# Optimization experiments

Hardware: AMD Instinct MI355X
Metric: run time of the kernel (lower is better)

Reference implementation:

```python
import jax, jax.numpy as jnp
import numpy as np

N_NODES = 100000
N_EDGES = 625000
D_IN = 128
D_OUT = 128


def setup_inputs() -> dict:
    key = jax.random.key(0)
    k1, k2, k3, k4 = jax.random.split(key, 4)
    embeds = jax.random.normal(k1, (N_NODES, D_IN), dtype=jnp.float32)
    weight = jax.random.normal(k2, (D_IN, D_OUT), dtype=jnp.float32)
    # COO sparse adjacency: row 0 = destination node, row 1 = source node
    edge_index = jax.random.randint(k3, (2, N_DGES := N_EDGES), 0, N_NODES, dtype=jnp.int32)
    edge_vals = jax.random.uniform(k4, (N_EDGES,), dtype=jnp.float32)
    return {"embeds": embeds, "weight": weight, "edge_index": edge_index, "edge_vals": edge_vals}


def reference(embeds, weight, edge_index, edge_vals):
    # support = embeds @ W  -> [N, D_OUT]
    support = jnp.matmul(embeds, weight)
    dst, src = edge_index[0], edge_index[1]
    # spmm: out[d] = sum_{e: dst[e]==d} vals[e] * support[src[e]]
    msgs = edge_vals[:, None] * support[src]  # [E, D_OUT]
    output = jax.ops.segment_sum(msgs, dst, num_segments=embeds.shape[0])
    return output
```

## Files before the change

kernel.cpp:

```cpp
#include <hip/hip_runtime.h>

#define D 128
#define CB 256
#define CB_SHIFT 8
#define NB_MAX 512
#define CAP 4096

typedef __attribute__((ext_vector_type(8))) short short8;
typedef __attribute__((ext_vector_type(4))) float f32x4;

__device__ inline ushort f2bf(float f) {
    uint u = __float_as_uint(f);
    uint r = (u + 0x7FFFu + ((u >> 16) & 1u)) >> 16;
    return (ushort)r;
}

__device__ inline uint cvtpk(float lo, float hi) {
    uint r;
    asm("v_cvt_pk_bf16_f32 %0, %1, %2" : "=v"(r) : "v"(lo), "v"(hi));
    return r;
}


__global__ __launch_bounds__(256) void init_kernel(int* __restrict__ cnt,
                                                   const float* __restrict__ W,
                                                   ushort* __restrict__ wT) {
    const int t = threadIdx.x;
    if (blockIdx.x == 0) { cnt[t] = 0; cnt[t + 256] = 0; }
    const int gt = blockIdx.x * 256 + t;
    if (gt < D * D) { int r = gt >> 7, c = gt & 127; wT[c * D + r] = f2bf(W[gt]); }
}


__global__ void zero_f4_kernel(float4* __restrict__ out, int n4) {
    int i = blockIdx.x * blockDim.x + threadIdx.x;
    int stride = gridDim.x * blockDim.x;
    float4 z = make_float4(0.f, 0.f, 0.f, 0.f);
    for (; i < n4; i += stride) out[i] = z;
}


__global__ __launch_bounds__(512) void gemm_part(const float* __restrict__ embeds,
                                                 const ushort* __restrict__ wT,
                                                 ushort* __restrict__ support, int N,
                                                 const int* __restrict__ dst,
                                                 const int* __restrict__ srcp,
                                                 const float* __restrict__ vals,
                                                 int* __restrict__ cnt,
                                                 int2* __restrict__ pay1, int E, int npart) {
    __shared__ ushort bLds[D * D];
    __shared__ int phist[NB_MAX];
    __shared__ int pbase[NB_MAX];
    const int t = threadIdx.x;

    if ((int)blockIdx.x < npart) {
        const int ntile = (E + 2047) >> 11;
        for (int tile = blockIdx.x; tile < ntile; tile += npart) {
            const int e0 = tile << 11;
            if (t < NB_MAX) phist[t] = 0;
            __syncthreads();

            int bk[4], rk[4];
            #pragma unroll
            for (int j = 0; j < 4; ++j) {
                int e = e0 + j * 512 + t;
                bk[j] = -1;
                if (e < E) {
                    bk[j] = dst[e] >> CB_SHIFT;
                    rk[j] = atomicAdd(&phist[bk[j]], 1);
                }
            }
            __syncthreads();

            if (t < NB_MAX)
                pbase[t] = phist[t] ? (t * CAP + atomicAdd(&cnt[t], phist[t])) : 0;
            __syncthreads();

            #pragma unroll
            for (int j = 0; j < 4; ++j) {
                int e = e0 + j * 512 + t;
                if (e >= E) continue;
                int d = dst[e];
                int pos = pbase[bk[j]] + rk[j];
                if (pos < (bk[j] + 1) * CAP) {
                    int key = ((d & (CB - 1)) << 17) | srcp[e];
                    pay1[pos] = make_int2(key, __float_as_int(vals[e]));
                }
            }
            __syncthreads();
        }
        return;
    }

    const int gbid = blockIdx.x - npart;
    const int ngemm = gridDim.x - npart;
    const int w = t >> 6;
    const int l = t & 63;
    const int kgrp = l >> 4;
    const int lan15 = l & 15;

    #pragma unroll
    for (int c = 0; c < 4; ++c) {
        int chunk = c * 512 + t;
        int byteoff = chunk * 16;
        int n = byteoff >> 8;
        int dstoff = byteoff ^ ((n & 7) << 4);
        *(float4*)((char*)bLds + dstoff) = *(const float4*)((const char*)wT + byteoff);
    }
    __syncthreads();

    const int ntiles = (N + 127) >> 7;

    for (int tile = gbid; tile < ntiles; tile += ngemm) {
        const int row0 = tile << 7;
        const int grow = row0 + w * 16 + lan15;
        const bool valid = grow < N;
        const float* arow = embeds + (size_t)grow * D + kgrp * 8;

        float4 pf[8];
        if (valid) {
            #pragma unroll
            for (int ks = 0; ks < 4; ++ks) {
                pf[2 * ks]     = *(const float4*)(arow + ks * 32);
                pf[2 * ks + 1] = *(const float4*)(arow + ks * 32 + 4);
            }
        } else {
            #pragma unroll
            for (int j = 0; j < 8; ++j) pf[j] = make_float4(0.f, 0.f, 0.f, 0.f);
        }

        f32x4 acc[8];
        #pragma unroll
        for (int ct = 0; ct < 8; ++ct) acc[ct] = (f32x4)0.0f;

        #pragma unroll
        for (int ks = 0; ks < 4; ++ks) {
            union { uint4 u; short8 s; } cv;
            const float4 f0 = pf[2 * ks], f1 = pf[2 * ks + 1];
            cv.u.x = cvtpk(f0.x, f0.y);
            cv.u.y = cvtpk(f0.z, f0.w);
            cv.u.z = cvtpk(f1.x, f1.y);
            cv.u.w = cvtpk(f1.z, f1.w);
            const short8 af = cv.s;

            const int kbyte = ks * 64 + kgrp * 16;
            #pragma unroll
            for (int ct = 0; ct < 8; ++ct) {
                const int n = ct * 16 + lan15;
                const int boff = (n * 256 + kbyte) ^ ((n & 7) << 4);
                short8 bfr = *(const short8*)((const char*)bLds + boff);
                acc[ct] = __builtin_amdgcn_mfma_f32_16x16x32_bf16(af, bfr, acc[ct], 0, 0, 0);
            }
        }

        #pragma unroll
        for (int r = 0; r < 4; ++r) {
            const int orow = row0 + w * 16 + kgrp * 4 + r;
            if (orow < N) {
                ushort* srow = &support[(size_t)orow * D + lan15];
                #pragma unroll
                for (int cp = 0; cp < 4; ++cp) {
                    uint u = cvtpk(acc[2 * cp][r], acc[2 * cp + 1][r]);
                    srow[(2 * cp) * 16] = (ushort)u;
                    srow[(2 * cp + 1) * 16] = (ushort)(u >> 16);
                }
            }
        }
    }
}


__global__ __launch_bounds__(256) void finefill2(const int2* __restrict__ pay1,
                                                 const int* __restrict__ cnt,
                                                 int2* __restrict__ ranges,
                                                 int2* __restrict__ pay,
                                                 int N, int nb) {
    __shared__ int lcnt[CB];
    __shared__ int bs[CB];
    __shared__ int lofs[CB];
    const int t = threadIdx.x;

    for (int b = blockIdx.x; b < nb; b += gridDim.x) {
        const int beg = b * CAP;
        const int end = beg + min(cnt[b], CAP);
        const int d0 = b << CB_SHIFT;

        lcnt[t] = 0;
        __syncthreads();
        for (int i = beg + t; i < end; i += 256)
            atomicAdd(&lcnt[((unsigned)pay1[i].x) >> 17], 1);
        __syncthreads();

        const int c = lcnt[t];
        bs[t] = c;
        __syncthreads();
        for (int off = 1; off < 256; off <<= 1) {
            int x = (t >= off) ? bs[t - off] : 0;
            __syncthreads();
            bs[t] += x;
            __syncthreads();
        }
        const int run = bs[t] - c + beg;
        if (d0 + t < N) ranges[d0 + t] = make_int2(run, run + c);
        lofs[t] = run;
        __syncthreads();

        for (int i = beg + t; i < end; i += 256) {
            int2 p = pay1[i];
            int dl = ((unsigned)p.x) >> 17;
            int pos = atomicAdd(&lofs[dl], 1);
            pay[pos] = make_int2(p.x & 0x1FFFF, p.y);
        }
        __syncthreads();
    }
}


#define EDGE_MAC(P, M)                                          \
    do {                                                        \
        const float v_ = __int_as_float((P).y);                 \
        acc[0] += v_ * __uint_as_float(((M).x & 0xFFFFu) << 16);\
        acc[1] += v_ * __uint_as_float((M).x & 0xFFFF0000u);    \
        acc[2] += v_ * __uint_as_float(((M).y & 0xFFFFu) << 16);\
        acc[3] += v_ * __uint_as_float((M).y & 0xFFFF0000u);    \
        acc[4] += v_ * __uint_as_float(((M).z & 0xFFFFu) << 16);\
        acc[5] += v_ * __uint_as_float((M).z & 0xFFFF0000u);    \
        acc[6] += v_ * __uint_as_float(((M).w & 0xFFFFu) << 16);\
        acc[7] += v_ * __uint_as_float((M).w & 0xFFFF0000u);    \
    } while (0)

__global__ __launch_bounds__(256, 8) void gather_kernel(const ushort* __restrict__ support,
                                                        const int2* __restrict__ ranges,
                                                        const int2* __restrict__ pay,
                                                        float* __restrict__ out, int N) {
    const int gid = (blockIdx.x * 256 + threadIdx.x) >> 4;
    const int sl = threadIdx.x & 15;
    if (gid >= N) return;

    const int2 rg = ranges[gid];
    const int beg = rg.x;
    const int end = rg.y;

    float acc[8];
    #pragma unroll
    for (int j = 0; j < 8; ++j) acc[j] = 0.f;

    int i = beg;
    for (; i + 3 < end; i += 4) {
        const int2 p0 = pay[i], p1 = pay[i + 1], p2 = pay[i + 2], p3 = pay[i + 3];
        const uint4 m0 = *(const uint4*)&support[(size_t)p0.x * D + sl * 8];
        const uint4 m1 = *(const uint4*)&support[(size_t)p1.x * D + sl * 8];
        const uint4 m2 = *(const uint4*)&support[(size_t)p2.x * D + sl * 8];
        const uint4 m3 = *(const uint4*)&support[(size_t)p3.x * D + sl * 8];
        EDGE_MAC(p0, m0); EDGE_MAC(p1, m1); EDGE_MAC(p2, m2); EDGE_MAC(p3, m3);
    }
    for (; i + 1 < end; i += 2) {
        const int2 p0 = pay[i], p1 = pay[i + 1];
        const uint4 m0 = *(const uint4*)&support[(size_t)p0.x * D + sl * 8];
        const uint4 m1 = *(const uint4*)&support[(size_t)p1.x * D + sl * 8];
        EDGE_MAC(p0, m0); EDGE_MAC(p1, m1);
    }
    if (i < end) {
        const int2 p0 = pay[i];
        const uint4 m0 = *(const uint4*)&support[(size_t)p0.x * D + sl * 8];
        EDGE_MAC(p0, m0);
    }

    float* o = &out[(size_t)gid * D + sl * 8];
    *(float4*)o       = make_float4(acc[0], acc[1], acc[2], acc[3]);
    *(float4*)(o + 4) = make_float4(acc[4], acc[5], acc[6], acc[7]);
}


__global__ __launch_bounds__(256) void scatter_kernel(const ushort* __restrict__ support,
                                                      const int* __restrict__ dst,
                                                      const int* __restrict__ src,
                                                      const float* __restrict__ vals,
                                                      float* __restrict__ out, int E) {
    const long long tid = (long long)blockIdx.x * blockDim.x + threadIdx.x;
    const int e = (int)(tid >> 6);
    if (e >= E) return;
    const int c = ((int)tid & 63) * 2;

    const int s = src[e];
    const int d = dst[e];
    const float v = vals[e];

    const uint m = *(const uint*)&support[(size_t)s * D + c];
    const float mx = __uint_as_float((m & 0xFFFFu) << 16);
    const float my = __uint_as_float(m & 0xFFFF0000u);
    atomicAdd(&out[(size_t)d * D + c + 0], v * mx);
    atomicAdd(&out[(size_t)d * D + c + 1], v * my);
}


static inline char* align256(char* p) {
    return (char*)(((uintptr_t)p + 255) & ~(uintptr_t)255);
}

extern "C" void kernel_launch(void* const* d_in, const int* in_sizes, int n_in,
                              void* d_out, int out_size, void* d_ws, size_t ws_size,
                              hipStream_t stream) {
    const float* embeds = (const float*)d_in[0];
    const float* W      = (const float*)d_in[1];
    const int*   eidx   = (const int*)d_in[2];
    const float* vals   = (const float*)d_in[3];

    const int N = in_sizes[0] / D;
    const int E = in_sizes[3];
    const int* dstp = eidx;
    const int* srcp = eidx + E;

    float* out = (float*)d_out;

    const int nb = (N + CB - 1) / CB;

    char* p = (char*)d_ws;
    ushort* support = (ushort*)p;  p = align256(p + (size_t)N * D * 2);
    ushort* wT      = (ushort*)p;  p = align256(p + (size_t)D * D * 2);
    int2* ranges    = (int2*)p;    p = align256(p + (size_t)N * 8);
    int* cnt        = (int*)p;     p = align256(p + NB_MAX * 4);
    int2* pay       = (int2*)p;    p = align256(p + (size_t)nb * CAP * 8);
    int2* pay1      = (int2*)p;    p = align256(p + (size_t)nb * CAP * 8);
    const size_t needed = (size_t)(p - (char*)d_ws);

    const bool two_level = (N <= (1 << 17)) && (nb <= NB_MAX) &&
                           ((long long)E * 2 <= (long long)nb * CAP) &&
                           (ws_size >= needed);

    if (two_level) {
        init_kernel<<<64, 256, 0, stream>>>(cnt, W, wT);

        const int ntile = (E + 2047) / 2048;
        const int npart = ntile < 512 ? ntile : 512;
        gemm_part<<<npart + 512, 512, 0, stream>>>(embeds, wT, support, N,
                                                   dstp, srcp, vals, cnt, pay1, E, npart);

        finefill2<<<nb, 256, 0, stream>>>(pay1, cnt, ranges, pay, N, nb);
        gather_kernel<<<(N * 16 + 255) / 256, 256, 0, stream>>>(support, ranges, pay, out, N);
    } else {
        init_kernel<<<64, 256, 0, stream>>>(cnt, W, wT);
        gemm_part<<<512, 512, 0, stream>>>(embeds, wT, support, N,
                                           dstp, srcp, vals, cnt, pay1, E, 0);
        zero_f4_kernel<<<2048, 256, 0, stream>>>((float4*)out, out_size / 4);
        const long long nthreads = (long long)E * 64;
        const int blocks = (int)((nthreads + 255) / 256);
        scatter_kernel<<<blocks, 256, 0, stream>>>(support, dstp, srcp, vals, out, E);
    }
}
```

Baseline: 74.62 us.

## Use one GEMM tile per block, larger partition tiles, and wider LDS swizzle

The GEMM blocks now each handle exactly one 128-row tile, launched as ntiles blocks, instead of grid-striding over tiles with 512 blocks. The partition phase processes 8192-edge tiles per block and takes slots through shared-memory atomics on pbase rather than keeping per-thread ranks in registers. The LDS swizzle for the weight matrix changes from a 3-bit to a 4-bit XOR pattern to cut bank conflicts. In exchange, each block now loads the full weight matrix into LDS for a single tile, and the slot order within a bucket becomes nondeterministic.

Result: no change. 74.59 us (-0.0%).

```diff
diff --git a/kernel.cpp b/kernel.cpp
--- a/kernel.cpp
+++ b/kernel.cpp
@@ -5,6 +5,7 @@
 #define CB_SHIFT 8
 #define NB_MAX 512
 #define CAP 4096
+#define PT 8192
 
 typedef __attribute__((ext_vector_type(8))) short short8;
 typedef __attribute__((ext_vector_type(4))) float f32x4;
@@ -54,36 +55,28 @@
     const int t = threadIdx.x;
 
     if ((int)blockIdx.x < npart) {
-        const int ntile = (E + 2047) >> 11;
+        const int ntile = (E + PT - 1) / PT;
         for (int tile = blockIdx.x; tile < ntile; tile += npart) {
-            const int e0 = tile << 11;
+            const int e0 = tile * PT;
+            const int e1 = min(e0 + PT, E);
+
             if (t < NB_MAX) phist[t] = 0;
             __syncthreads();
 
-            int bk[4], rk[4];
-            #pragma unroll
-            for (int j = 0; j < 4; ++j) {
-                int e = e0 + j * 512 + t;
-                bk[j] = -1;
-                if (e < E) {
-                    bk[j] = dst[e] >> CB_SHIFT;
-                    rk[j] = atomicAdd(&phist[bk[j]], 1);
-                }
-            }
+            for (int e = e0 + t; e < e1; e += 512)
+                atomicAdd(&phist[dst[e] >> CB_SHIFT], 1);
             __syncthreads();
 
             if (t < NB_MAX)
                 pbase[t] = phist[t] ? (t * CAP + atomicAdd(&cnt[t], phist[t])) : 0;
             __syncthreads();
 
-            #pragma unroll
-            for (int j = 0; j < 4; ++j) {
-                int e = e0 + j * 512 + t;
-                if (e >= E) continue;
-                int d = dst[e];
-                int pos = pbase[bk[j]] + rk[j];
-                if (pos < (bk[j] + 1) * CAP) {
-                    int key = ((d & (CB - 1)) << 17) | srcp[e];
+            for (int e = e0 + t; e < e1; e += 512) {
+                const int d = dst[e];
+                const int b = d >> CB_SHIFT;
+                const int pos = atomicAdd(&pbase[b], 1);
+                if (pos < (b + 1) * CAP) {
+                    const int key = ((d & (CB - 1)) << 17) | srcp[e];
                     pay1[pos] = make_int2(key, __float_as_int(vals[e]));
                 }
             }
@@ -92,8 +85,10 @@
         return;
     }
 
-    const int gbid = blockIdx.x - npart;
-    const int ngemm = gridDim.x - npart;
+    const int tile = blockIdx.x - npart;
+    const int ntiles = (N + 127) >> 7;
+    if (tile >= ntiles) return;
+
     const int w = t >> 6;
     const int l = t & 63;
     const int kgrp = l >> 4;
@@ -104,66 +99,62 @@
         int chunk = c * 512 + t;
         int byteoff = chunk * 16;
         int n = byteoff >> 8;
-        int dstoff = byteoff ^ ((n & 7) << 4);
+        int dstoff = byteoff ^ ((n & 15) << 4);
         *(float4*)((char*)bLds + dstoff) = *(const float4*)((const char*)wT + byteoff);
     }
     __syncthreads();
 
-    const int ntiles = (N + 127) >> 7;
-
-    for (int tile = gbid; tile < ntiles; tile += ngemm) {
-        const int row0 = tile << 7;
-        const int grow = row0 + w * 16 + lan15;
-        const bool valid = grow < N;
-        const float* arow = embeds + (size_t)grow * D + kgrp * 8;
-
-        float4 pf[8];
-        if (valid) {
-            #pragma unroll
-            for (int ks = 0; ks < 4; ++ks) {
-                pf[2 * ks]     = *(const float4*)(arow + ks * 32);
-                pf[2 * ks + 1] = *(const float4*)(arow + ks * 32 + 4);
-            }
-        } else {
-            #pragma unroll
-            for (int j = 0; j < 8; ++j) pf[j] = make_float4(0.f, 0.f, 0.f, 0.f);
-        }
-
-        f32x4 acc[8];
-        #pragma unroll
-        for (int ct = 0; ct < 8; ++ct) acc[ct] = (f32x4)0.0f;
-
+    const int row0 = tile << 7;
+    const int grow = row0 + w * 16 + lan15;
+    const bool valid = grow < N;
+    const float* arow = embeds + (size_t)grow * D + kgrp * 8;
+
+    float4 pf[8];
+    if (valid) {
         #pragma unroll
         for (int ks = 0; ks < 4; ++ks) {
-            union { uint4 u; short8 s; } cv;
-            const float4 f0 = pf[2 * ks], f1 = pf[2 * ks + 1];
-            cv.u.x = cvtpk(f0.x, f0.y);
-            cv.u.y = cvtpk(f0.z, f0.w);
-            cv.u.z = cvtpk(f1.x, f1.y);
-            cv.u.w = cvtpk(f1.z, f1.w);
-            const short8 af = cv.s;
-
-            const int kbyte = ks * 64 + kgrp * 16;
+            pf[2 * ks]     = *(const float4*)(arow + ks * 32);
+            pf[2 * ks + 1] = *(const float4*)(arow + ks * 32 + 4);
+        }
+    } else {
+        #pragma unroll
+        for (int j = 0; j < 8; ++j) pf[j] = make_float4(0.f, 0.f, 0.f, 0.f);
+    }
+
+    f32x4 acc[8];
+    #pragma unroll
+    for (int ct = 0; ct < 8; ++ct) acc[ct] = (f32x4)0.0f;
+
+    #pragma unroll
+    for (int ks = 0; ks < 4; ++ks) {
+        union { uint4 u; short8 s; } cv;
+        const float4 f0 = pf[2 * ks], f1 = pf[2 * ks + 1];
+        cv.u.x = cvtpk(f0.x, f0.y);
+        cv.u.y = cvtpk(f0.z, f0.w);
+        cv.u.z = cvtpk(f1.x, f1.y);
+        cv.u.w = cvtpk(f1.z, f1.w);
+        const short8 af = cv.s;
+
+        const int kbyte = ks * 64 + kgrp * 16;
+        #pragma unroll
+        for (int ct = 0; ct < 8; ++ct) {
+            const int n = ct * 16 + lan15;
+            const int boff = (n * 256 + kbyte) ^ ((n & 15) << 4);
+            short8 bfr = *(const short8*)((const char*)bLds + boff);
+            acc[ct] = __builtin_amdgcn_mfma_f32_16x16x32_bf16(af, bfr, acc[ct], 0, 0, 0);
+        }
+    }
+
+    #pragma unroll
+    for (int r = 0; r < 4; ++r) {
+        const int orow = row0 + w * 16 + kgrp * 4 + r;
+        if (orow < N) {
+            ushort* srow = &support[(size_t)orow * D + lan15];
             #pragma unroll
-            for (int ct = 0; ct < 8; ++ct) {
-                const int n = ct * 16 + lan15;
-                const int boff = (n * 256 + kbyte) ^ ((n & 7) << 4);
-                short8 bfr = *(const short8*)((const char*)bLds + boff);
-                acc[ct] = __builtin_amdgcn_mfma_f32_16x16x32_bf16(af, bfr, acc[ct], 0, 0, 0);
-            }
-        }
-
-        #pragma unroll
-        for (int r = 0; r < 4; ++r) {
-            const int orow = row0 + w * 16 + kgrp * 4 + r;
-            if (orow < N) {
-                ushort* srow = &support[(size_t)orow * D + lan15];
-                #pragma unroll
-                for (int cp = 0; cp < 4; ++cp) {
-                    uint u = cvtpk(acc[2 * cp][r], acc[2 * cp + 1][r]);
-                    srow[(2 * cp) * 16] = (ushort)u;
-                    srow[(2 * cp + 1) * 16] = (ushort)(u >> 16);
-                }
+            for (int cp = 0; cp < 4; ++cp) {
+                uint u = cvtpk(acc[2 * cp][r], acc[2 * cp + 1][r]);
+                srow[(2 * cp) * 16] = (ushort)u;
+                srow[(2 * cp + 1) * 16] = (ushort)(u >> 16);
             }
         }
     }
@@ -314,6 +305,7 @@
     float* out = (float*)d_out;
 
     const int nb = (N + CB - 1) / CB;
+    const int ntiles = (N + 127) >> 7;
 
     char* p = (char*)d_ws;
     ushort* support = (ushort*)p;  p = align256(p + (size_t)N * D * 2);
@@ -331,17 +323,19 @@
     if (two_level) {
         init_kernel<<<64, 256, 0, stream>>>(cnt, W, wT);
 
-        const int ntile = (E + 2047) / 2048;
-        const int npart = ntile < 512 ? ntile : 512;
-        gemm_part<<<npart + 512, 512, 0, stream>>>(embeds, wT, support, N,
-                                                   dstp, srcp, vals, cnt, pay1, E, npart);
+        const int ptile = (E + PT - 1) / PT;
+        const int npart = ptile < 512 ? ptile : 512;
+        int total = npart + ntiles;
+        if (total > 1024 && npart + 512 < total) total = (npart + ntiles);
+        gemm_part<<<npart + ntiles, 512, 0, stream>>>(embeds, wT, support, N,
+                                                      dstp, srcp, vals, cnt, pay1, E, npart);
 
         finefill2<<<nb, 256, 0, stream>>>(pay1, cnt, ranges, pay, N, nb);
         gather_kernel<<<(N * 16 + 255) / 256, 256, 0, stream>>>(support, ranges, pay, out, N);
     } else {
         init_kernel<<<64, 256, 0, stream>>>(cnt, W, wT);
-        gemm_part<<<512, 512, 0, stream>>>(embeds, wT, support, N,
-                                           dstp, srcp, vals, cnt, pay1, E, 0);
+        gemm_part<<<ntiles, 512, 0, stream>>>(embeds, wT, support, N,
+                                              dstp, srcp, vals, cnt, pay1, E, 0);
         zero_f4_kernel<<<2048, 256, 0, stream>>>((float4*)out, out_size / 4);
         const long long nthreads = (long long)E * 64;
         const int blocks = (int)((nthreads + 255) / 256);
```

## Split fused GEMM/partition kernel into separate partition and one-tile-per-block GEMM kernels

Applied to the files above, without the earlier changes.

Replaces the combined gemm_part launch, where some blocks partitioned edges and others ran persistent GEMM loops, with two kernels launched back to back: a 256-thread partition kernel with one block per tile, and a GEMM kernel with one block per 128-row tile. The LDS swizzle for the weight tile also changes from an XOR over 8 rows to one over 16 rows, to cut bank conflicts. The GEMM blocks no longer run beside the partition work. In exchange there is an extra launch, and each GEMM block now reloads the weight tile into LDS.

Result: slower. 80.90 us (+8.4%).

```diff
diff --git a/kernel.cpp b/kernel.cpp
--- a/kernel.cpp
+++ b/kernel.cpp
@@ -5,6 +5,7 @@
 #define CB_SHIFT 8
 #define NB_MAX 512
 #define CAP 4096
+#define PT 2048
 
 typedef __attribute__((ext_vector_type(8))) short short8;
 typedef __attribute__((ext_vector_type(4))) float f32x4;
@@ -40,60 +41,64 @@
 }
 
 
-__global__ __launch_bounds__(512) void gemm_part(const float* __restrict__ embeds,
-                                                 const ushort* __restrict__ wT,
-                                                 ushort* __restrict__ support, int N,
-                                                 const int* __restrict__ dst,
-                                                 const int* __restrict__ srcp,
-                                                 const float* __restrict__ vals,
-                                                 int* __restrict__ cnt,
-                                                 int2* __restrict__ pay1, int E, int npart) {
-    __shared__ ushort bLds[D * D];
+__global__ __launch_bounds__(256) void part_kernel(const int* __restrict__ dst,
+                                                   const int* __restrict__ srcp,
+                                                   const float* __restrict__ vals,
+                                                   int* __restrict__ cnt,
+                                                   int2* __restrict__ pay1, int E) {
     __shared__ int phist[NB_MAX];
     __shared__ int pbase[NB_MAX];
     const int t = threadIdx.x;
-
-    if ((int)blockIdx.x < npart) {
-        const int ntile = (E + 2047) >> 11;
-        for (int tile = blockIdx.x; tile < ntile; tile += npart) {
-            const int e0 = tile << 11;
-            if (t < NB_MAX) phist[t] = 0;
-            __syncthreads();
-
-            int bk[4], rk[4];
-            #pragma unroll
-            for (int j = 0; j < 4; ++j) {
-                int e = e0 + j * 512 + t;
-                bk[j] = -1;
-                if (e < E) {
-                    bk[j] = dst[e] >> CB_SHIFT;
-                    rk[j] = atomicAdd(&phist[bk[j]], 1);
-                }
+    const int ntile = (E + PT - 1) / PT;
+
+    for (int tile = blockIdx.x; tile < ntile; tile += gridDim.x) {
+        const int e0 = tile * PT;
+        #pragma unroll
+        for (int j = t; j < NB_MAX; j += 256) phist[j] = 0;
+        __syncthreads();
+
+        int bk[8], rk[8];
+        #pragma unroll
+        for (int j = 0; j < 8; ++j) {
+            int e = e0 + j * 256 + t;
+            bk[j] = -1;
+            if (e < E) {
+                bk[j] = dst[e] >> CB_SHIFT;
+                rk[j] = atomicAdd(&phist[bk[j]], 1);
             }
-            __syncthreads();
-
-            if (t < NB_MAX)
-                pbase[t] = phist[t] ? (t * CAP + atomicAdd(&cnt[t], phist[t])) : 0;
-            __syncthreads();
-
-            #pragma unroll
-            for (int j = 0; j < 4; ++j) {
-                int e = e0 + j * 512 + t;
-                if (e >= E) continue;
-                int d = dst[e];
-                int pos = pbase[bk[j]] + rk[j];
-                if (pos < (bk[j] + 1) * CAP) {
-                    int key = ((d & (CB - 1)) << 17) | srcp[e];
-                    pay1[pos] = make_int2(key, __float_as_int(vals[e]));
-                }
+        }
+        __syncthreads();
+
+        #pragma unroll
+        for (int j = t; j < NB_MAX; j += 256)
+            pbase[j] = phist[j] ? (j * CAP + atomicAdd(&cnt[j], phist[j])) : 0;
+        __syncthreads();
+
+        #pragma unroll
+        for (int j = 0; j < 8; ++j) {
+            int e = e0 + j * 256 + t;
+            if (e >= E) continue;
+            int d = dst[e];
+            int pos = pbase[bk[j]] + rk[j];
+            if (pos < (bk[j] + 1) * CAP) {
+                int key = ((d & (CB - 1)) << 17) | srcp[e];
+                pay1[pos] = make_int2(key, __float_as_int(vals[e]));
             }
-            __syncthreads();
-        }
-        return;
-    }
-
-    const int gbid = blockIdx.x - npart;
-    const int ngemm = gridDim.x - npart;
+        }
+        __syncthreads();
+    }
+}
+
+
+__global__ __launch_bounds__(512) void gemm_kernel(const float* __restrict__ embeds,
+                                                   const ushort* __restrict__ wT,
+                                                   ushort* __restrict__ support, int N) {
+    __shared__ ushort bLds[D * D];
+    const int t = threadIdx.x;
+    const int tile = blockIdx.x;
+    const int ntiles = (N + 127) >> 7;
+    if (tile >= ntiles) return;
+
     const int w = t >> 6;
     const int l = t & 63;
     const int kgrp = l >> 4;
@@ -104,66 +109,62 @@
         int chunk = c * 512 + t;
         int byteoff = chunk * 16;
         int n = byteoff >> 8;
-        int dstoff = byteoff ^ ((n & 7) << 4);
+        int dstoff = byteoff ^ ((n & 15) << 4);
         *(float4*)((char*)bLds + dstoff) = *(const float4*)((const char*)wT + byteoff);
     }
     __syncthreads();
 
-    const int ntiles = (N + 127) >> 7;
-
-    for (int tile = gbid; tile < ntiles; tile += ngemm) {
-        const int row0 = tile << 7;
-        const int grow = row0 + w * 16 + lan15;
-        const bool valid = grow < N;
-        const float* arow = embeds + (size_t)grow * D + kgrp * 8;
-
-        float4 pf[8];
-        if (valid) {
+    const int row0 = tile << 7;
+    const int grow = row0 + w * 16 + lan15;
+    const bool valid = grow < N;
+    const float* arow = embeds + (size_t)grow * D + kgrp * 8;
+
+    float4 pf[8];
+    if (valid) {
+        #pragma unroll
+        for (int ks = 0; ks < 4; ++ks) {
+            pf[2 * ks]     = *(const float4*)(arow + ks * 32);
+            pf[2 * ks + 1] = *(const float4*)(arow + ks * 32 + 4);
+        }
+    } else {
+        #pragma unroll
+        for (int j = 0; j < 8; ++j) pf[j] = make_float4(0.f, 0.f, 0.f, 0.f);
+    }
+
+    f32x4 acc[8];
+    #pragma unroll
+    for (int ct = 0; ct < 8; ++ct) acc[ct] = (f32x4)0.0f;
+
+    #pragma unroll
+    for (int ks = 0; ks < 4; ++ks) {
+        union { uint4 u; short8 s; } cv;
+        const float4 f0 = pf[2 * ks], f1 = pf[2 * ks + 1];
+        cv.u.x = cvtpk(f0.x, f0.y);
+        cv.u.y = cvtpk(f0.z, f0.w);
+        cv.u.z = cvtpk(f1.x, f1.y);
+        cv.u.w = cvtpk(f1.z, f1.w);
+        const short8 af = cv.s;
+
+        const int kbyte = ks * 64 + kgrp * 16;
+        #pragma unroll
+        for (int ct = 0; ct < 8; ++ct) {
+            const int n = ct * 16 + lan15;
+            const int boff = (n * 256 + kbyte) ^ ((n & 15) << 4);
+            short8 bfr = *(const short8*)((const char*)bLds + boff);
+            acc[ct] = __builtin_amdgcn_mfma_f32_16x16x32_bf16(af, bfr, acc[ct], 0, 0, 0);
+        }
+    }
+
+    #pragma unroll
+    for (int r = 0; r < 4; ++r) {
+        const int orow = row0 + w * 16 + kgrp * 4 + r;
+        if (orow < N) {
+            ushort* srow = &support[(size_t)orow * D + lan15];
             #pragma unroll
-            for (int ks = 0; ks < 4; ++ks) {
-                pf[2 * ks]     = *(const float4*)(arow + ks * 32);
-                pf[2 * ks + 1] = *(const float4*)(arow + ks * 32 + 4);
-            }
-        } else {
-            #pragma unroll
-            for (int j = 0; j < 8; ++j) pf[j] = make_float4(0.f, 0.f, 0.f, 0.f);
-        }
-
-        f32x4 acc[8];
-        #pragma unroll
-        for (int ct = 0; ct < 8; ++ct) acc[ct] = (f32x4)0.0f;
-
-        #pragma unroll
-        for (int ks = 0; ks < 4; ++ks) {
-            union { uint4 u; short8 s; } cv;
-            const float4 f0 = pf[2 * ks], f1 = pf[2 * ks + 1];
-            cv.u.x = cvtpk(f0.x, f0.y);
-            cv.u.y = cvtpk(f0.z, f0.w);
-            cv.u.z = cvtpk(f1.x, f1.y);
-            cv.u.w = cvtpk(f1.z, f1.w);
-            const short8 af = cv.s;
-
-            const int kbyte = ks * 64 + kgrp * 16;
-            #pragma unroll
-            for (int ct = 0; ct < 8; ++ct) {
-                const int n = ct * 16 + lan15;
-                const int boff = (n * 256 + kbyte) ^ ((n & 7) << 4);
-                short8 bfr = *(const short8*)((const char*)bLds + boff);
-                acc[ct] = __builtin_amdgcn_mfma_f32_16x16x32_bf16(af, bfr, acc[ct], 0, 0, 0);
-            }
-        }
-
-        #pragma unroll
-        for (int r = 0; r < 4; ++r) {
-            const int orow = row0 + w * 16 + kgrp * 4 + r;
-            if (orow < N) {
-                ushort* srow = &support[(size_t)orow * D + lan15];
-                #pragma unroll
-                for (int cp = 0; cp < 4; ++cp) {
-                    uint u = cvtpk(acc[2 * cp][r], acc[2 * cp + 1][r]);
-                    srow[(2 * cp) * 16] = (ushort)u;
-                    srow[(2 * cp + 1) * 16] = (ushort)(u >> 16);
-                }
+            for (int cp = 0; cp < 4; ++cp) {
+                uint u = cvtpk(acc[2 * cp][r], acc[2 * cp + 1][r]);
+                srow[(2 * cp) * 16] = (ushort)u;
+                srow[(2 * cp + 1) * 16] = (ushort)(u >> 16);
             }
         }
     }
@@ -314,6 +315,7 @@
     float* out = (float*)d_out;
 
     const int nb = (N + CB - 1) / CB;
+    const int ntiles = (N + 127) >> 7;
 
     char* p = (char*)d_ws;
     ushort* support = (ushort*)p;  p = align256(p + (size_t)N * D * 2);
@@ -331,17 +333,14 @@
     if (two_level) {
         init_kernel<<<64, 256, 0, stream>>>(cnt, W, wT);
 
-        const int ntile = (E + 2047) / 2048;
-        const int npart = ntile < 512 ? ntile : 512;
-        gemm_part<<<npart + 512, 512, 0, stream>>>(embeds, wT, support, N,
-                                                   dstp, srcp, vals, cnt, pay1, E, npart);
-
+        const int ptile = (E + PT - 1) / PT;
+        part_kernel<<<ptile, 256, 0, stream>>>(dstp, srcp, vals, cnt, pay1, E);
+        gemm_kernel<<<ntiles, 512, 0, stream>>>(embeds, wT, support, N);
         finefill2<<<nb, 256, 0, stream>>>(pay1, cnt, ranges, pay, N, nb);
         gather_kernel<<<(N * 16 + 255) / 256, 256, 0, stream>>>(support, ranges, pay, out, N);
     } else {
         init_kernel<<<64, 256, 0, stream>>>(cnt, W, wT);
-        gemm_part<<<512, 512, 0, stream>>>(embeds, wT, support, N,
-                                           dstp, srcp, vals, cnt, pay1, E, 0);
+        gemm_kernel<<<ntiles, 512, 0, stream>>>(embeds, wT, support, N);
         zero_f4_kernel<<<2048, 256, 0, stream>>>((float4*)out, out_size / 4);
         const long long nthreads = (long long)E * 64;
         const int blocks = (int)((nthreads + 255) / 256);
```
